# Kernel tuning notes

Measured on AMD Instinct MI355X. Metric: run time of the kernel, lower is better.

Reference implementation:

```python
import jax, jax.numpy as jnp
import numpy as np

T = 4096        # sequence length
D = 128         # input feature dim
TRACE = 64      # trace_size
CONTEXT = 64    # context_size
HID = 64        # internal dense width (hardcoded 64 in module)
OUT = 128       # output_size
LN_EPS = 1e-6   # flax LayerNorm default epsilon


def setup_inputs() -> dict:
    key = jax.random.key(0)
    ks = jax.random.split(key, 12)

    def dense(k, fi, fo):
        return (jax.random.normal(k, (fi, fo), jnp.float32) / np.sqrt(fi).astype(np.float32))

    inp = {}
    inp["x"] = jax.random.normal(ks[0], (T, D), jnp.float32)
    inp["state"] = jnp.zeros((1, TRACE, CONTEXT), jnp.complex64)
    inp["start"] = jax.random.uniform(ks[1], (T,)) < 0.01  # sparse episode resets
    # deterministic FFM decay / frequency params (init_deterministic)
    inp["a"] = jnp.linspace(1e-6, 0.5, TRACE).astype(jnp.float32)
    inp["b"] = (2.0 * jnp.pi / jnp.linspace(1.0, 1000.0, CONTEXT)).astype(jnp.float32)
    inp["W1"] = dense(ks[2], D, HID);               inp["b1"] = jnp.zeros((HID,), jnp.float32)
    inp["W2"] = dense(ks[3], HID, 2 * TRACE);       inp["b2"] = jnp.zeros((2 * TRACE,), jnp.float32)
    inp["Wgi"] = dense(ks[4], 2 * TRACE, TRACE);    inp["bgi"] = jnp.zeros((TRACE,), jnp.float32)
    inp["Wp"] = dense(ks[5], 2 * TRACE, TRACE);     inp["bp"] = jnp.zeros((TRACE,), jnp.float32)
    inp["Wz"] = dense(ks[6], 2 * TRACE * CONTEXT, HID); inp["bz"] = jnp.zeros((HID,), jnp.float32)
    inp["Wgo"] = dense(ks[7], 2 * TRACE, HID);      inp["bgo"] = jnp.zeros((HID,), jnp.float32)
    inp["Ws"] = dense(ks[8], 2 * TRACE, HID);       inp["bs"] = jnp.zeros((HID,), jnp.float32)
    inp["W3"] = dense(ks[9], HID, HID);             inp["b3"] = jnp.zeros((HID,), jnp.float32)
    inp["W4"] = dense(ks[10], HID, OUT);            inp["b4"] = jnp.zeros((OUT,), jnp.float32)
    return inp


def _ffm_scan(scan_in, state0, start, a, b):
    # scan_in: (T, TRACE, CONTEXT) float, state0: (1, TRACE, CONTEXT) complex64
    t = scan_in.shape[0]
    timestep = jnp.ones((t + 1, 1, 1), dtype=jnp.int32)
    start_f = jnp.concatenate(
        [jnp.zeros((1, 1, 1), dtype=bool), start.reshape(t, 1, 1)], axis=0)
    xs = jnp.concatenate([state0, scan_in.astype(jnp.complex64)], axis=0)

    neg_a = -jnp.abs(a).reshape(1, TRACE, 1)
    b_r = b.reshape(1, 1, CONTEXT)
    ab = neg_a + 1j * b_r  # (1, TRACE, CONTEXT) complex

    def gamma(j):
        # j: (N,1,1) int -> (N, TRACE, CONTEXT) complex decay
        return jnp.exp(ab * j.astype(jnp.float32))

    def combine(carry, incoming):
        prev_start, s, i = carry
        st, xx, j = incoming
        keep = jnp.logical_not(st)
        s = s * keep
        j = j * keep.astype(j.dtype)
        new_s = s * gamma(j) + xx
        return (jnp.logical_or(st, prev_start), new_s, j + i)

    _, new_state, _ = jax.lax.associative_scan(
        combine, (start_f, xs, timestep), axis=0)
    return new_state[1:]  # (T, TRACE, CONTEXT) complex64


def _layernorm(x):
    mu = jnp.mean(x, axis=-1, keepdims=True)
    var = jnp.var(x, axis=-1, keepdims=True)
    return (x - mu) * jax.lax.rsqrt(var + LN_EPS)


def _forward(x, state, start, a, b, W1, b1, W2, b2, Wgi, bgi, Wp, bp,
             Wz, bz, Wgo, bgo, Ws, bs, W3, b3, W4, b4):
    h = jax.nn.relu(x @ W1 + b1)                 # (T, 64)
    h2 = h @ W2 + b2                             # (T, 2*TRACE)
    gate_in = jax.nn.sigmoid(h2 @ Wgi + bgi)     # (T, TRACE)
    pre = jax.nn.sigmoid(h2 @ Wp + bp)           # (T, TRACE)
    gated = pre * gate_in                        # (T, TRACE)
    scan_in = jnp.broadcast_to(gated[:, :, None], (gated.shape[0], TRACE, CONTEXT))
    state_seq = _ffm_scan(scan_in, state, start, a, b)  # (T, TRACE, CONTEXT) c64
    z_in = jnp.concatenate([jnp.real(state_seq), jnp.imag(state_seq)],
                           axis=-1).reshape(state_seq.shape[0], -1)
    z = z_in @ Wz + bz                           # (T, 64)
    gate_out = jax.nn.sigmoid(h2 @ Wgo + bgo)    # (T, 64)
    skip = h2 @ Ws + bs                          # (T, 64)
    out = _layernorm(z * gate_out) + skip * (1.0 - gate_out)
    out = jax.nn.relu(out @ W3 + b3)
    out = out @ W4 + b4                          # (T, OUT)
    return out, state_seq[-1:]


def reference(x, state, start, a, b, W1, b1, W2, b2, Wgi, bgi, Wp, bp,
              Wz, bz, Wgo, bgo, Ws, bs, W3, b3, W4, b4):
    return _forward(x, state, start, a, b, W1, b1, W2, b2, Wgi, bgi, Wp, bp,
                    Wz, bz, Wgo, bgo, Ws, bs, W3, b3, W4, b4)
```

## Files before the change

### kernel.cpp

```cpp
#include <hip/hip_runtime.h>
#include <math.h>

#define T_LEN 4096
#define D_IN 128
#define HID 64
#define KDIM 4096
#define K2   8192

#define OFF_GATED 0u
#define OFF_GO    262144u
#define OFF_SKIP  524288u
#define OFF_PART  786432u
#define OFF_FLAGS 4980736u
#define OFF_CHS   4984832u
#define OFF_WZT   4984896u
#define OFF_SCR   5247040u

typedef __attribute__((ext_vector_type(8))) short short8v;
typedef __attribute__((ext_vector_type(4))) float float4v;

__device__ __forceinline__ float sigm(float x){ return 1.f/(1.f+expf(-x)); }
__device__ __forceinline__ unsigned short f2bf(float x){
    unsigned int u = __float_as_uint(x);
    return (unsigned short)((u + 0x7FFFu + ((u >> 16) & 1u)) >> 16);
}

__global__ __launch_bounds__(512) void k_prep(
    const unsigned char* __restrict__ su8, const int* __restrict__ si32,
    int* __restrict__ flags, int* __restrict__ chunkStart,
    const float* __restrict__ Wz, unsigned short* __restrict__ wzt,
    const float* __restrict__ x,
    const float* __restrict__ W1, const float* __restrict__ b1,
    const float* __restrict__ W2, const float* __restrict__ b2,
    const float* __restrict__ Wgi, const float* __restrict__ bgi,
    const float* __restrict__ Wp,  const float* __restrict__ bp,
    const float* __restrict__ Wgo, const float* __restrict__ bgo,
    const float* __restrict__ Wsk, const float* __restrict__ bsk,
    float* __restrict__ gated, float* __restrict__ go, float* __restrict__ sk)
{
    const int bx = blockIdx.x;
    const int tid = threadIdx.x;

    if (bx == 0) {
        __shared__ int cnt;
        if (tid == 0) cnt = 0;
        __syncthreads();
        int local = 0;
        for (int i = tid; i < 4096; i += 512)
            if (i & 3) local += su8[i];
        if (local) atomicAdd(&cnt, local);
        __syncthreads();
        if (cnt > 0) {
            for (int i = tid; i < 4096; i += 512) flags[i] = su8[i] ? 1 : 0;
        } else {
            for (int i = tid; i < 4096; i += 512) flags[i] = si32[i] ? 1 : 0;
        }
        __syncthreads();
        if (tid < 64) {
            int any = 0;
#pragma unroll 8
            for (int j = 0; j < 64; ++j) any |= flags[tid * 64 + j];
            chunkStart[tid] = any;
        }
        return;
    }
    if (bx <= 64) {
        int idx = ((bx - 1) * 512 + tid) * 16;
        int j = idx >> 13, k0 = idx & 8191;
#pragma unroll
        for (int e = 0; e < 16; ++e) {
            int k = k0 + e;
            wzt[(size_t)j * K2 + k] = f2bf(Wz[(size_t)k * 64 + j]);
        }
        return;
    }

    __shared__ float xs[8][128];
    __shared__ float hs[8][64];
    __shared__ float h2s[8][128];
    __shared__ float tmp[8][4][64];
    const int t0 = (bx - 65) * 8;

    if (tid < 256) {
        int r = tid >> 5, kq = (tid & 31) << 2;
        *(float4*)&xs[r][kq] = *(const float4*)&x[(size_t)(t0 + r) * D_IN + kq];
    }

    const int j1 = tid >> 3, ks1 = tid & 7;
    float wr1[16];
#pragma unroll
    for (int kk = 0; kk < 16; ++kk) wr1[kk] = W1[(size_t)(ks1 * 16 + kk) * HID + j1];
    const float bias1 = b1[j1];
    __syncthreads();
#pragma unroll
    for (int r = 0; r < 8; ++r) {
        float p = 0.f;
#pragma unroll
        for (int kq = 0; kq < 4; ++kq) {
            float4 xv = *(const float4*)&xs[r][ks1 * 16 + kq * 4];
            p += xv.x * wr1[kq*4] + xv.y * wr1[kq*4+1] + xv.z * wr1[kq*4+2] + xv.w * wr1[kq*4+3];
        }
        p += __shfl_xor(p, 1, 64); p += __shfl_xor(p, 2, 64); p += __shfl_xor(p, 4, 64);
        if (ks1 == 0) hs[r][j1] = fmaxf(p + bias1, 0.f);
    }

    const int j2 = tid >> 2, ks2 = tid & 3;
    float wr2[16];
#pragma unroll
    for (int kk = 0; kk < 16; ++kk) wr2[kk] = W2[(size_t)(ks2 * 16 + kk) * 128 + j2];
    const float bias2 = b2[j2];
    __syncthreads();
#pragma unroll
    for (int r = 0; r < 8; ++r) {
        float p = 0.f;
#pragma unroll
        for (int kq = 0; kq < 4; ++kq) {
            float4 hv = *(const float4*)&hs[r][ks2 * 16 + kq * 4];
            p += hv.x * wr2[kq*4] + hv.y * wr2[kq*4+1] + hv.z * wr2[kq*4+2] + hv.w * wr2[kq*4+3];
        }
        p += __shfl_xor(p, 1, 64); p += __shfl_xor(p, 2, 64);
        if (ks2 == 0) h2s[r][j2] = p + bias2;
    }

    const int mat = tid >> 7, jj = (tid & 127) >> 1, kh = tid & 1;
    const float* Wm = (mat == 0) ? Wgi : (mat == 1) ? Wp : (mat == 2) ? Wgo : Wsk;
    float wgr[64];
#pragma unroll
    for (int kk = 0; kk < 64; ++kk) wgr[kk] = Wm[(size_t)(kh * 64 + kk) * 64 + jj];
    __syncthreads();
#pragma unroll
    for (int r = 0; r < 8; ++r) {
        float p = 0.f;
#pragma unroll
        for (int kq = 0; kq < 16; ++kq) {
            float4 hv = *(const float4*)&h2s[r][kh * 64 + kq * 4];
            p += hv.x * wgr[kq*4] + hv.y * wgr[kq*4+1] + hv.z * wgr[kq*4+2] + hv.w * wgr[kq*4+3];
        }
        p += __shfl_xor(p, 1, 64);
        if (kh == 0) tmp[r][mat][jj] = p;
    }
    __syncthreads();

    {
        int r = tid >> 6, j = tid & 63;
        int t = t0 + r;
        float gi = sigm(tmp[r][0][j] + bgi[j]);
        float pr = sigm(tmp[r][1][j] + bp[j]);
        float g  = sigm(tmp[r][2][j] + bgo[j]);
        float s  = tmp[r][3][j] + bsk[j];
        gated[t * 64 + j] = gi * pr;
        go[t * 64 + j]    = g;
        sk[t * 64 + j]    = s;
    }
}

__global__ __launch_bounds__(512) void k_scanA(
    const float* __restrict__ gated, const int* __restrict__ flags,
    const float* __restrict__ a, const float* __restrict__ b,
    float2* __restrict__ carryB)
{
    const int p = threadIdx.x >> 6, c = threadIdx.x & 63;
    const int pair = blockIdx.x * 8 + p;
    const int ch = pair & 63, m = pair >> 6;
    const int t0 = ch * 64;
    __shared__ float gb[8][64];
    __shared__ int fb[8][64];
    gb[p][c] = gated[(size_t)(t0 + c) * 64 + m];
    fb[p][c] = flags[t0 + c];
    __syncthreads();

    const double ea = exp(-fabs((double)a[m]));
    const double bb = (double)b[c];
    const double lre = ea * cos(bb), lim = ea * sin(bb);
    double sre = 0.0, sim = 0.0;
#pragma unroll 8
    for (int j = 0; j < 64; ++j) {
        double g = (double)gb[p][j];
        if (fb[p][j]) { sre = g; sim = 0.0; }
        else {
            double nr = fma(sre, lre, fma(-sim, lim, g));
            double ni = fma(sre, lim, sim * lre);
            sre = nr; sim = ni;
        }
    }
    carryB[(size_t)ch * KDIM + m * 64 + c] = make_float2((float)sre, (float)sim);
}

__global__ __launch_bounds__(64) void k_scanC(
    const float2* __restrict__ carryB, const int* __restrict__ chunkStart,
    const float* __restrict__ a, const float* __restrict__ b,
    const float* __restrict__ st0,
    float2* __restrict__ cinArr)
{
    const int m = blockIdx.x, c = threadIdx.x;
    __shared__ int chsS[64];
    chsS[c] = chunkStart[c];

    float2 Bv[64];
#pragma unroll
    for (int ch = 0; ch < 64; ++ch)
        Bv[ch] = carryB[(size_t)ch * KDIM + m * 64 + c];
    __syncthreads();

    const double ea64 = exp(-64.0 * fabs((double)a[m]));
    const double bb = (double)b[c];
    const double l64re = ea64 * cos(64.0 * bb), l64im = ea64 * sin(64.0 * bb);
    double cre = (double)st0[(m * 64 + c) * 2];
    double cim = (double)st0[(m * 64 + c) * 2 + 1];
#pragma unroll
    for (int ch = 0; ch < 64; ++ch) {
        cinArr[(size_t)ch * KDIM + m * 64 + c] = make_float2((float)cre, (float)cim);
        if (chsS[ch]) { cre = (double)Bv[ch].x; cim = (double)Bv[ch].y; }
        else {
            double nr = fma(cre, l64re, fma(-cim, l64im, (double)Bv[ch].x));
            double ni = fma(cre, l64im, fma(cim, l64re, (double)Bv[ch].y));
            cre = nr; cim = ni;
        }
    }
}

__global__ __launch_bounds__(256) void k_scanBZ(
    const float* __restrict__ gated, const int* __restrict__ flags,
    const float* __restrict__ a, const float* __restrict__ b,
    const float2* __restrict__ cinArr,
    const unsigned short* __restrict__ wzt,
    float* __restrict__ part,
    float* __restrict__ out)
{
    const int tid = threadIdx.x;
    const int ml = tid >> 6, c = tid & 63;
    const int ch = blockIdx.x & 63, mg = blockIdx.x >> 6;
    const int m = mg * 4 + ml;
    const int t0 = ch * 64;
    __shared__ unsigned short st[64 * 512];
    __shared__ float gb[4][64];
    __shared__ int fb[64];
    gb[ml][c] = gated[(size_t)(t0 + c) * 64 + m];
    if (ml == 0) fb[c] = flags[t0 + c];
    __syncthreads();

    const double ea = exp(-fabs((double)a[m]));
    const double bb = (double)b[c];
    const double lre = ea * cos(bb), lim = ea * sin(bb);
    float2 cin = cinArr[(size_t)ch * KDIM + m * 64 + c];
    double sre = (double)cin.x, sim = (double)cin.y;
    const int e0 = ml * 128 + c, e1 = ml * 128 + 64 + c;
#pragma unroll 4
    for (int j = 0; j < 64; ++j) {
        double g = (double)gb[ml][j];
        if (fb[j]) { sre = g; sim = 0.0; }
        else {
            double nr = fma(sre, lre, fma(-sim, lim, g));
            double ni = fma(sre, lim, sim * lre);
            sre = nr; sim = ni;
        }
        const int sx = (j & 7) << 3;
        st[j * 512 + (e0 ^ sx)] = f2bf((float)sre);
        st[j * 512 + (e1 ^ sx)] = f2bf((float)sim);
    }
    if (ch == 63) {
        out[524288 + m * 64 + c]        = (float)sre;
        out[524288 + 4096 + m * 64 + c] = (float)sim;
    }

    const int l = c;
    const int jrow = ml * 16 + (l & 15);
    short8v bfr[16];
#pragma unroll
    for (int ks = 0; ks < 16; ++ks)
        bfr[ks] = *(const short8v*)&wzt[(size_t)jrow * K2 + mg * 512 + (ks * 4 + (l >> 4)) * 8];

    __syncthreads();

    float4v acc[4];
#pragma unroll
    for (int i = 0; i < 4; ++i) acc[i] = (float4v){0.f, 0.f, 0.f, 0.f};
#pragma unroll
    for (int ks = 0; ks < 16; ++ks) {
#pragma unroll
        for (int mt = 0; mt < 4; ++mt) {
            const int row = mt * 16 + (l & 15);
            const int rchunk = (ks * 4 + (l >> 4)) ^ (row & 7);
            short8v af = *(const short8v*)&st[row * 512 + rchunk * 8];
            acc[mt] = __builtin_amdgcn_mfma_f32_16x16x32_bf16(af, bfr[ks], acc[mt], 0, 0, 0);
        }
    }

    float* pp = part + (size_t)mg * 262144;
    const int jcol = ml * 16 + (l & 15);
#pragma unroll
    for (int mt = 0; mt < 4; ++mt) {
        const int trow = t0 + mt * 16 + (l >> 4) * 4;
#pragma unroll
        for (int r = 0; r < 4; ++r)
            pp[(size_t)(trow + r) * 64 + jcol] = acc[mt][r];
    }
}

__device__ __forceinline__ float wsum(float v) {
#pragma unroll
    for (int o = 32; o; o >>= 1) v += __shfl_xor(v, o, 64);
    return v;
}

__global__ __launch_bounds__(256) void k_epi(
    const float* __restrict__ part, const float* __restrict__ bz,
    const float* __restrict__ go, const float* __restrict__ sk,
    const float* __restrict__ W3, const float* __restrict__ b3,
    const float* __restrict__ W4, const float* __restrict__ b4,
    float* __restrict__ out)
{
    __shared__ float ob[4][64], hb[4][64];
    const int w = threadIdx.x >> 6, j = threadIdx.x & 63;
    const int t = blockIdx.x * 4 + w;
    float z = bz[j];
#pragma unroll
    for (int p = 0; p < 16; ++p) z += part[(size_t)p * 262144 + t * 64 + j];
    float g = go[t * 64 + j];
    float y = z * g;
    float mu = wsum(y) * 0.015625f;
    float d = y - mu;
    float var = wsum(d * d) * 0.015625f;
    float o = d * (1.f / sqrtf(var + 1e-6f)) + sk[t * 64 + j] * (1.f - g);
    ob[w][j] = o;
    __syncthreads();
    float acc = b3[j];
#pragma unroll 8
    for (int k = 0; k < 64; ++k) acc += ob[w][k] * W3[k * 64 + j];
    hb[w][j] = fmaxf(acc, 0.f);
    __syncthreads();
    float o1 = b4[j], o2 = b4[j + 64];
#pragma unroll 8
    for (int k = 0; k < 64; ++k) { float hv = hb[w][k]; o1 += hv * W4[k * 128 + j]; o2 += hv * W4[k * 128 + j + 64]; }
    out[(size_t)t * 128 + j] = o1;
    out[(size_t)t * 128 + j + 64] = o2;
}

extern "C" void kernel_launch(void* const* d_in, const int* in_sizes, int n_in,
                              void* d_out, int out_size, void* d_ws, size_t ws_size,
                              hipStream_t stream)
{
    const float* x   = (const float*)d_in[0];
    const float* st0 = (const float*)d_in[1];
    const void*  start = d_in[2];
    const float* a  = (const float*)d_in[3];
    const float* b  = (const float*)d_in[4];
    const float* W1 = (const float*)d_in[5];  const float* b1 = (const float*)d_in[6];
    const float* W2 = (const float*)d_in[7];  const float* b2 = (const float*)d_in[8];
    const float* Wgi= (const float*)d_in[9];  const float* bgi= (const float*)d_in[10];
    const float* Wp = (const float*)d_in[11]; const float* bp = (const float*)d_in[12];
    const float* Wz = (const float*)d_in[13]; const float* bz = (const float*)d_in[14];
    const float* Wgo= (const float*)d_in[15]; const float* bgo= (const float*)d_in[16];
    const float* Wsk= (const float*)d_in[17]; const float* bsk= (const float*)d_in[18];
    const float* W3 = (const float*)d_in[19]; const float* b3 = (const float*)d_in[20];
    const float* W4 = (const float*)d_in[21]; const float* b4 = (const float*)d_in[22];

    float* ws    = (float*)d_ws;
    float* out   = (float*)d_out;
    float* gated = ws + OFF_GATED;
    float* go    = ws + OFF_GO;
    float* sk    = ws + OFF_SKIP;
    float* part  = ws + OFF_PART;
    int*   flags = (int*)(ws + OFF_FLAGS);
    int*   chs   = (int*)(ws + OFF_CHS);
    unsigned short* wzt  = (unsigned short*)(ws + OFF_WZT);

    float2* carryB = (float2*)(ws + OFF_SCR);
    float2* cinArr = (float2*)(ws + OFF_SCR + 524288);

    hipLaunchKernelGGL(k_prep, dim3(577), dim3(512), 0, stream,
                       (const unsigned char*)start, (const int*)start, flags, chs,
                       Wz, wzt, x, W1, b1, W2, b2, Wgi, bgi, Wp, bp,
                       Wgo, bgo, Wsk, bsk, gated, go, sk);
    hipLaunchKernelGGL(k_scanA, dim3(512), dim3(512), 0, stream,
                       gated, flags, a, b, carryB);
    hipLaunchKernelGGL(k_scanC, dim3(64), dim3(64), 0, stream,
                       carryB, chs, a, b, st0, cinArr);
    hipLaunchKernelGGL(k_scanBZ, dim3(1024), dim3(256), 0, stream,
                       gated, flags, a, b, cinArr, wzt, part, out);
    hipLaunchKernelGGL(k_epi, dim3(1024), dim3(256), 0, stream,
                       part, bz, go, sk, W3, b3, W4, b4, out);
}
```

Before: 86.17 us.

## Fuse five kernels into one persistent kernel with global atomic barriers

```diff
diff --git a/kernel.cpp b/kernel.cpp
--- a/kernel.cpp
+++ b/kernel.cpp
@@ -3,9 +3,9 @@
 
 #define T_LEN 4096
 #define D_IN 128
-#define HID 64
 #define KDIM 4096
 #define K2   8192
+#define NBLK 256
 
 #define OFF_GATED 0u
 #define OFF_GO    262144u
@@ -15,6 +15,7 @@
 #define OFF_CHS   4984832u
 #define OFF_WZT   4984896u
 #define OFF_SCR   5247040u
+#define OFF_BAR   6295616u
 
 typedef __attribute__((ext_vector_type(8))) short short8v;
 typedef __attribute__((ext_vector_type(4))) float float4v;
@@ -24,360 +25,327 @@
     unsigned int u = __float_as_uint(x);
     return (unsigned short)((u + 0x7FFFu + ((u >> 16) & 1u)) >> 16);
 }
-
-__global__ __launch_bounds__(512) void k_prep(
-    const unsigned char* __restrict__ su8, const int* __restrict__ si32,
-    int* __restrict__ flags, int* __restrict__ chunkStart,
-    const float* __restrict__ Wz, unsigned short* __restrict__ wzt,
-    const float* __restrict__ x,
-    const float* __restrict__ W1, const float* __restrict__ b1,
-    const float* __restrict__ W2, const float* __restrict__ b2,
-    const float* __restrict__ Wgi, const float* __restrict__ bgi,
-    const float* __restrict__ Wp,  const float* __restrict__ bp,
-    const float* __restrict__ Wgo, const float* __restrict__ bgo,
-    const float* __restrict__ Wsk, const float* __restrict__ bsk,
-    float* __restrict__ gated, float* __restrict__ go, float* __restrict__ sk)
-{
+__device__ __forceinline__ float wsum(float v) {
+#pragma unroll
+    for (int o = 32; o; o >>= 1) v += __shfl_xor(v, o, 64);
+    return v;
+}
+
+struct Params {
+    const unsigned char* su8; const int* si32;
+    const float *x, *st0, *a, *b;
+    const float *W1,*b1,*W2,*b2,*Wgi,*bgi,*Wp,*bp,*Wz,*bz,*Wgo,*bgo,*Wsk,*bsk,*W3,*b3,*W4,*b4;
+    float *gated,*go,*sk,*part; int *flags,*chs; unsigned short* wzt;
+    float2 *carryB,*cinArr; float* out; int* bar;
+};
+
+__device__ __forceinline__ void gsync(int* bar) {
+    __syncthreads();
+    if (threadIdx.x == 0) {
+        __threadfence();
+        atomicAdd(bar, 1);
+        while (atomicAdd(bar, 0) < NBLK) __builtin_amdgcn_s_sleep(8);
+        __threadfence();
+    }
+    __syncthreads();
+}
+
+__global__ __launch_bounds__(512) void k_mega(Params P) {
+    __shared__ __align__(16) char smem[65536];
     const int bx = blockIdx.x;
     const int tid = threadIdx.x;
 
     if (bx == 0) {
-        __shared__ int cnt;
-        if (tid == 0) cnt = 0;
+        int* cnt = (int*)(smem + 20480);
+        if (tid == 0) *cnt = 0;
         __syncthreads();
         int local = 0;
         for (int i = tid; i < 4096; i += 512)
-            if (i & 3) local += su8[i];
-        if (local) atomicAdd(&cnt, local);
+            if (i & 3) local += P.su8[i];
+        if (local) atomicAdd(cnt, local);
         __syncthreads();
-        if (cnt > 0) {
-            for (int i = tid; i < 4096; i += 512) flags[i] = su8[i] ? 1 : 0;
-        } else {
-            for (int i = tid; i < 4096; i += 512) flags[i] = si32[i] ? 1 : 0;
-        }
+        if (*cnt > 0) { for (int i = tid; i < 4096; i += 512) P.flags[i] = P.su8[i] ? 1 : 0; }
+        else          { for (int i = tid; i < 4096; i += 512) P.flags[i] = P.si32[i] ? 1 : 0; }
         __syncthreads();
         if (tid < 64) {
             int any = 0;
 #pragma unroll 8
-            for (int j = 0; j < 64; ++j) any |= flags[tid * 64 + j];
-            chunkStart[tid] = any;
-        }
-        return;
-    }
-    if (bx <= 64) {
+            for (int j = 0; j < 64; ++j) any |= P.flags[tid * 64 + j];
+            P.chs[tid] = any;
+        }
+    }
+    if (bx >= 1 && bx <= 64) {
         int idx = ((bx - 1) * 512 + tid) * 16;
         int j = idx >> 13, k0 = idx & 8191;
 #pragma unroll
         for (int e = 0; e < 16; ++e) {
             int k = k0 + e;
-            wzt[(size_t)j * K2 + k] = f2bf(Wz[(size_t)k * 64 + j]);
-        }
-        return;
-    }
-
-    __shared__ float xs[8][128];
-    __shared__ float hs[8][64];
-    __shared__ float h2s[8][128];
-    __shared__ float tmp[8][4][64];
-    const int t0 = (bx - 65) * 8;
-
-    if (tid < 256) {
-        int r = tid >> 5, kq = (tid & 31) << 2;
-        *(float4*)&xs[r][kq] = *(const float4*)&x[(size_t)(t0 + r) * D_IN + kq];
-    }
-
-    const int j1 = tid >> 3, ks1 = tid & 7;
-    float wr1[16];
-#pragma unroll
-    for (int kk = 0; kk < 16; ++kk) wr1[kk] = W1[(size_t)(ks1 * 16 + kk) * HID + j1];
-    const float bias1 = b1[j1];
-    __syncthreads();
-#pragma unroll
-    for (int r = 0; r < 8; ++r) {
-        float p = 0.f;
-#pragma unroll
-        for (int kq = 0; kq < 4; ++kq) {
-            float4 xv = *(const float4*)&xs[r][ks1 * 16 + kq * 4];
-            p += xv.x * wr1[kq*4] + xv.y * wr1[kq*4+1] + xv.z * wr1[kq*4+2] + xv.w * wr1[kq*4+3];
-        }
-        p += __shfl_xor(p, 1, 64); p += __shfl_xor(p, 2, 64); p += __shfl_xor(p, 4, 64);
-        if (ks1 == 0) hs[r][j1] = fmaxf(p + bias1, 0.f);
-    }
-
-    const int j2 = tid >> 2, ks2 = tid & 3;
-    float wr2[16];
-#pragma unroll
-    for (int kk = 0; kk < 16; ++kk) wr2[kk] = W2[(size_t)(ks2 * 16 + kk) * 128 + j2];
-    const float bias2 = b2[j2];
-    __syncthreads();
-#pragma unroll
-    for (int r = 0; r < 8; ++r) {
-        float p = 0.f;
-#pragma unroll
-        for (int kq = 0; kq < 4; ++kq) {
-            float4 hv = *(const float4*)&hs[r][ks2 * 16 + kq * 4];
-            p += hv.x * wr2[kq*4] + hv.y * wr2[kq*4+1] + hv.z * wr2[kq*4+2] + hv.w * wr2[kq*4+3];
-        }
-        p += __shfl_xor(p, 1, 64); p += __shfl_xor(p, 2, 64);
-        if (ks2 == 0) h2s[r][j2] = p + bias2;
-    }
-
-    const int mat = tid >> 7, jj = (tid & 127) >> 1, kh = tid & 1;
-    const float* Wm = (mat == 0) ? Wgi : (mat == 1) ? Wp : (mat == 2) ? Wgo : Wsk;
-    float wgr[64];
-#pragma unroll
-    for (int kk = 0; kk < 64; ++kk) wgr[kk] = Wm[(size_t)(kh * 64 + kk) * 64 + jj];
-    __syncthreads();
-#pragma unroll
-    for (int r = 0; r < 8; ++r) {
-        float p = 0.f;
-#pragma unroll
-        for (int kq = 0; kq < 16; ++kq) {
-            float4 hv = *(const float4*)&h2s[r][kh * 64 + kq * 4];
-            p += hv.x * wgr[kq*4] + hv.y * wgr[kq*4+1] + hv.z * wgr[kq*4+2] + hv.w * wgr[kq*4+3];
-        }
-        p += __shfl_xor(p, 1, 64);
-        if (kh == 0) tmp[r][mat][jj] = p;
-    }
-    __syncthreads();
-
+            P.wzt[(size_t)j * K2 + k] = f2bf(P.Wz[(size_t)k * 64 + j]);
+        }
+    }
     {
-        int r = tid >> 6, j = tid & 63;
-        int t = t0 + r;
-        float gi = sigm(tmp[r][0][j] + bgi[j]);
-        float pr = sigm(tmp[r][1][j] + bp[j]);
-        float g  = sigm(tmp[r][2][j] + bgo[j]);
-        float s  = tmp[r][3][j] + bsk[j];
-        gated[t * 64 + j] = gi * pr;
-        go[t * 64 + j]    = g;
-        sk[t * 64 + j]    = s;
-    }
-}
-
-__global__ __launch_bounds__(512) void k_scanA(
-    const float* __restrict__ gated, const int* __restrict__ flags,
-    const float* __restrict__ a, const float* __restrict__ b,
-    float2* __restrict__ carryB)
-{
-    const int p = threadIdx.x >> 6, c = threadIdx.x & 63;
-    const int pair = blockIdx.x * 8 + p;
-    const int ch = pair & 63, m = pair >> 6;
-    const int t0 = ch * 64;
-    __shared__ float gb[8][64];
-    __shared__ int fb[8][64];
-    gb[p][c] = gated[(size_t)(t0 + c) * 64 + m];
-    fb[p][c] = flags[t0 + c];
-    __syncthreads();
-
-    const double ea = exp(-fabs((double)a[m]));
-    const double bb = (double)b[c];
-    const double lre = ea * cos(bb), lim = ea * sin(bb);
-    double sre = 0.0, sim = 0.0;
+        float (*xs)[128]  = (float(*)[128])smem;
+        float (*hs)[64]   = (float(*)[64])(smem + 4096);
+        float (*h2s)[128] = (float(*)[128])(smem + 6144);
+        float (*tmp)[4][64] = (float(*)[4][64])(smem + 10240);
+
+        const int j1 = tid >> 3, ks1 = tid & 7;
+        float wr1[16];
+#pragma unroll
+        for (int kk = 0; kk < 16; ++kk) wr1[kk] = P.W1[(size_t)(ks1 * 16 + kk) * 64 + j1];
+        const float bias1 = P.b1[j1];
+        const int j2 = tid >> 2, ks2 = tid & 3;
+        float wr2[16];
+#pragma unroll
+        for (int kk = 0; kk < 16; ++kk) wr2[kk] = P.W2[(size_t)(ks2 * 16 + kk) * 128 + j2];
+        const float bias2 = P.b2[j2];
+        const int mat = tid >> 7, jj = (tid & 127) >> 1, kh = tid & 1;
+        const float* Wm = (mat == 0) ? P.Wgi : (mat == 1) ? P.Wp : (mat == 2) ? P.Wgo : P.Wsk;
+        float wgr[64];
+#pragma unroll
+        for (int kk = 0; kk < 64; ++kk) wgr[kk] = Wm[(size_t)(kh * 64 + kk) * 64 + jj];
+
+        for (int u = 0; u < 2; ++u) {
+            const int t0 = (bx * 2 + u) * 8;
+            __syncthreads();
+            if (tid < 256) {
+                int r = tid >> 5, kq = (tid & 31) << 2;
+                *(float4*)&xs[r][kq] = *(const float4*)&P.x[(size_t)(t0 + r) * D_IN + kq];
+            }
+            __syncthreads();
+#pragma unroll
+            for (int r = 0; r < 8; ++r) {
+                float p = 0.f;
+#pragma unroll
+                for (int kq = 0; kq < 4; ++kq) {
+                    float4 xv = *(const float4*)&xs[r][ks1 * 16 + kq * 4];
+                    p += xv.x*wr1[kq*4] + xv.y*wr1[kq*4+1] + xv.z*wr1[kq*4+2] + xv.w*wr1[kq*4+3];
+                }
+                p += __shfl_xor(p, 1, 64); p += __shfl_xor(p, 2, 64); p += __shfl_xor(p, 4, 64);
+                if (ks1 == 0) hs[r][j1] = fmaxf(p + bias1, 0.f);
+            }
+            __syncthreads();
+#pragma unroll
+            for (int r = 0; r < 8; ++r) {
+                float p = 0.f;
+#pragma unroll
+                for (int kq = 0; kq < 4; ++kq) {
+                    float4 hv = *(const float4*)&hs[r][ks2 * 16 + kq * 4];
+                    p += hv.x*wr2[kq*4] + hv.y*wr2[kq*4+1] + hv.z*wr2[kq*4+2] + hv.w*wr2[kq*4+3];
+                }
+                p += __shfl_xor(p, 1, 64); p += __shfl_xor(p, 2, 64);
+                if (ks2 == 0) h2s[r][j2] = p + bias2;
+            }
+            __syncthreads();
+#pragma unroll
+            for (int r = 0; r < 8; ++r) {
+                float p = 0.f;
+#pragma unroll
+                for (int kq = 0; kq < 16; ++kq) {
+                    float4 hv = *(const float4*)&h2s[r][kh * 64 + kq * 4];
+                    p += hv.x*wgr[kq*4] + hv.y*wgr[kq*4+1] + hv.z*wgr[kq*4+2] + hv.w*wgr[kq*4+3];
+                }
+                p += __shfl_xor(p, 1, 64);
+                if (kh == 0) tmp[r][mat][jj] = p;
+            }
+            __syncthreads();
+            {
+                int r = tid >> 6, j = tid & 63;
+                int t = t0 + r;
+                float gi = sigm(tmp[r][0][j] + P.bgi[j]);
+                float pr = sigm(tmp[r][1][j] + P.bp[j]);
+                float g  = sigm(tmp[r][2][j] + P.bgo[j]);
+                float s  = tmp[r][3][j] + P.bsk[j];
+                P.gated[t * 64 + j] = gi * pr;
+                P.go[t * 64 + j]    = g;
+                P.sk[t * 64 + j]    = s;
+            }
+        }
+    }
+    gsync(P.bar + 0);
+
+    {
+        const int p = tid >> 6, c = tid & 63;
+#pragma unroll
+        for (int u = 0; u < 2; ++u) {
+            const int pair = (bx * 2 + u) * 8 + p;
+            const int ch = pair & 63, m = pair >> 6, t0s = ch * 64;
+            const double ea = exp(-fabs((double)P.a[m]));
+            const double bb = (double)P.b[c];
+            const double lre = ea * cos(bb), lim = ea * sin(bb);
+            float gv = P.gated[(size_t)(t0s + c) * 64 + m];
+            unsigned long long fmask = __ballot(P.flags[t0s + c] != 0);
+            double sre = 0.0, sim = 0.0;
 #pragma unroll 8
-    for (int j = 0; j < 64; ++j) {
-        double g = (double)gb[p][j];
-        if (fb[p][j]) { sre = g; sim = 0.0; }
-        else {
-            double nr = fma(sre, lre, fma(-sim, lim, g));
-            double ni = fma(sre, lim, sim * lre);
-            sre = nr; sim = ni;
-        }
-    }
-    carryB[(size_t)ch * KDIM + m * 64 + c] = make_float2((float)sre, (float)sim);
-}
-
-__global__ __launch_bounds__(64) void k_scanC(
-    const float2* __restrict__ carryB, const int* __restrict__ chunkStart,
-    const float* __restrict__ a, const float* __restrict__ b,
-    const float* __restrict__ st0,
-    float2* __restrict__ cinArr)
-{
-    const int m = blockIdx.x, c = threadIdx.x;
-    __shared__ int chsS[64];
-    chsS[c] = chunkStart[c];
-
-    float2 Bv[64];
-#pragma unroll
-    for (int ch = 0; ch < 64; ++ch)
-        Bv[ch] = carryB[(size_t)ch * KDIM + m * 64 + c];
-    __syncthreads();
-
-    const double ea64 = exp(-64.0 * fabs((double)a[m]));
-    const double bb = (double)b[c];
-    const double l64re = ea64 * cos(64.0 * bb), l64im = ea64 * sin(64.0 * bb);
-    double cre = (double)st0[(m * 64 + c) * 2];
-    double cim = (double)st0[(m * 64 + c) * 2 + 1];
-#pragma unroll
-    for (int ch = 0; ch < 64; ++ch) {
-        cinArr[(size_t)ch * KDIM + m * 64 + c] = make_float2((float)cre, (float)cim);
-        if (chsS[ch]) { cre = (double)Bv[ch].x; cim = (double)Bv[ch].y; }
-        else {
-            double nr = fma(cre, l64re, fma(-cim, l64im, (double)Bv[ch].x));
-            double ni = fma(cre, l64im, fma(cim, l64re, (double)Bv[ch].y));
-            cre = nr; cim = ni;
-        }
-    }
-}
-
-__global__ __launch_bounds__(256) void k_scanBZ(
-    const float* __restrict__ gated, const int* __restrict__ flags,
-    const float* __restrict__ a, const float* __restrict__ b,
-    const float2* __restrict__ cinArr,
-    const unsigned short* __restrict__ wzt,
-    float* __restrict__ part,
-    float* __restrict__ out)
-{
-    const int tid = threadIdx.x;
-    const int ml = tid >> 6, c = tid & 63;
-    const int ch = blockIdx.x & 63, mg = blockIdx.x >> 6;
-    const int m = mg * 4 + ml;
-    const int t0 = ch * 64;
-    __shared__ unsigned short st[64 * 512];
-    __shared__ float gb[4][64];
-    __shared__ int fb[64];
-    gb[ml][c] = gated[(size_t)(t0 + c) * 64 + m];
-    if (ml == 0) fb[c] = flags[t0 + c];
-    __syncthreads();
-
-    const double ea = exp(-fabs((double)a[m]));
-    const double bb = (double)b[c];
-    const double lre = ea * cos(bb), lim = ea * sin(bb);
-    float2 cin = cinArr[(size_t)ch * KDIM + m * 64 + c];
-    double sre = (double)cin.x, sim = (double)cin.y;
-    const int e0 = ml * 128 + c, e1 = ml * 128 + 64 + c;
+            for (int j = 0; j < 64; ++j) {
+                double g = (double)__shfl(gv, j, 64);
+                if ((fmask >> j) & 1) { sre = g; sim = 0.0; }
+                else {
+                    double nr = fma(sre, lre, fma(-sim, lim, g));
+                    double ni = fma(sre, lim, sim * lre);
+                    sre = nr; sim = ni;
+                }
+            }
+            P.carryB[(size_t)ch * KDIM + m * 64 + c] = make_float2((float)sre, (float)sim);
+        }
+    }
+    gsync(P.bar + 16);
+
+    if (bx < 64 && tid < 64) {
+        const int m = bx, c = tid;
+        unsigned long long cmask = __ballot(P.chs[c] != 0);
+        float2 Bv[64];
+#pragma unroll
+        for (int ch = 0; ch < 64; ++ch)
+            Bv[ch] = P.carryB[(size_t)ch * KDIM + m * 64 + c];
+        const double ea64 = exp(-64.0 * fabs((double)P.a[m]));
+        const double bb = (double)P.b[c];
+        const double l64re = ea64 * cos(64.0 * bb), l64im = ea64 * sin(64.0 * bb);
+        double cre = (double)P.st0[(m * 64 + c) * 2];
+        double cim = (double)P.st0[(m * 64 + c) * 2 + 1];
+#pragma unroll
+        for (int ch = 0; ch < 64; ++ch) {
+            P.cinArr[(size_t)ch * KDIM + m * 64 + c] = make_float2((float)cre, (float)cim);
+            if ((cmask >> ch) & 1) { cre = (double)Bv[ch].x; cim = (double)Bv[ch].y; }
+            else {
+                double nr = fma(cre, l64re, fma(-cim, l64im, (double)Bv[ch].x));
+                double ni = fma(cre, l64im, fma(cim, l64re, (double)Bv[ch].y));
+                cre = nr; cim = ni;
+            }
+        }
+    }
+    gsync(P.bar + 32);
+
+    {
+        unsigned short* st = (unsigned short*)smem;
+        const int w = tid >> 6, l = tid & 63;
+        const int ml = w & 3, mth = w >> 2;
+        for (int u = 0; u < 4; ++u) {
+            const int pair = bx * 4 + u;
+            const int ch = pair & 63, mg = pair >> 6, t0s = ch * 64;
+            const int m = mg * 4 + ml;
+            const int jrow = ml * 16 + (l & 15);
+            short8v bfr[16];
+#pragma unroll
+            for (int ks = 0; ks < 16; ++ks)
+                bfr[ks] = *(const short8v*)&P.wzt[(size_t)jrow * K2 + mg * 512 + (ks * 4 + (l >> 4)) * 8];
+            __syncthreads();
+            if (w < 4) {
+                const double ea = exp(-fabs((double)P.a[m]));
+                const double bb = (double)P.b[l];
+                const double lre = ea * cos(bb), lim = ea * sin(bb);
+                float gv = P.gated[(size_t)(t0s + l) * 64 + m];
+                unsigned long long fmask = __ballot(P.flags[t0s + l] != 0);
+                float2 cin = P.cinArr[(size_t)ch * KDIM + m * 64 + l];
+                double sre = (double)cin.x, sim = (double)cin.y;
+                const int e0 = ml * 128 + l, e1 = e0 + 64;
 #pragma unroll 4
-    for (int j = 0; j < 64; ++j) {
-        double g = (double)gb[ml][j];
-        if (fb[j]) { sre = g; sim = 0.0; }
-        else {
-            double nr = fma(sre, lre, fma(-sim, lim, g));
-            double ni = fma(sre, lim, sim * lre);
-            sre = nr; sim = ni;
-        }
-        const int sx = (j & 7) << 3;
-        st[j * 512 + (e0 ^ sx)] = f2bf((float)sre);
-        st[j * 512 + (e1 ^ sx)] = f2bf((float)sim);
-    }
-    if (ch == 63) {
-        out[524288 + m * 64 + c]        = (float)sre;
-        out[524288 + 4096 + m * 64 + c] = (float)sim;
-    }
-
-    const int l = c;
-    const int jrow = ml * 16 + (l & 15);
-    short8v bfr[16];
-#pragma unroll
-    for (int ks = 0; ks < 16; ++ks)
-        bfr[ks] = *(const short8v*)&wzt[(size_t)jrow * K2 + mg * 512 + (ks * 4 + (l >> 4)) * 8];
-
-    __syncthreads();
-
-    float4v acc[4];
-#pragma unroll
-    for (int i = 0; i < 4; ++i) acc[i] = (float4v){0.f, 0.f, 0.f, 0.f};
-#pragma unroll
-    for (int ks = 0; ks < 16; ++ks) {
-#pragma unroll
-        for (int mt = 0; mt < 4; ++mt) {
-            const int row = mt * 16 + (l & 15);
-            const int rchunk = (ks * 4 + (l >> 4)) ^ (row & 7);
-            short8v af = *(const short8v*)&st[row * 512 + rchunk * 8];
-            acc[mt] = __builtin_amdgcn_mfma_f32_16x16x32_bf16(af, bfr[ks], acc[mt], 0, 0, 0);
-        }
-    }
-
-    float* pp = part + (size_t)mg * 262144;
-    const int jcol = ml * 16 + (l & 15);
-#pragma unroll
-    for (int mt = 0; mt < 4; ++mt) {
-        const int trow = t0 + mt * 16 + (l >> 4) * 4;
-#pragma unroll
-        for (int r = 0; r < 4; ++r)
-            pp[(size_t)(trow + r) * 64 + jcol] = acc[mt][r];
-    }
-}
-
-__device__ __forceinline__ float wsum(float v) {
-#pragma unroll
-    for (int o = 32; o; o >>= 1) v += __shfl_xor(v, o, 64);
-    return v;
-}
-
-__global__ __launch_bounds__(256) void k_epi(
-    const float* __restrict__ part, const float* __restrict__ bz,
-    const float* __restrict__ go, const float* __restrict__ sk,
-    const float* __restrict__ W3, const float* __restrict__ b3,
-    const float* __restrict__ W4, const float* __restrict__ b4,
-    float* __restrict__ out)
-{
-    __shared__ float ob[4][64], hb[4][64];
-    const int w = threadIdx.x >> 6, j = threadIdx.x & 63;
-    const int t = blockIdx.x * 4 + w;
-    float z = bz[j];
-#pragma unroll
-    for (int p = 0; p < 16; ++p) z += part[(size_t)p * 262144 + t * 64 + j];
-    float g = go[t * 64 + j];
-    float y = z * g;
-    float mu = wsum(y) * 0.015625f;
-    float d = y - mu;
-    float var = wsum(d * d) * 0.015625f;
-    float o = d * (1.f / sqrtf(var + 1e-6f)) + sk[t * 64 + j] * (1.f - g);
-    ob[w][j] = o;
-    __syncthreads();
-    float acc = b3[j];
+                for (int j = 0; j < 64; ++j) {
+                    double g = (double)__shfl(gv, j, 64);
+                    if ((fmask >> j) & 1) { sre = g; sim = 0.0; }
+                    else {
+                        double nr = fma(sre, lre, fma(-sim, lim, g));
+                        double ni = fma(sre, lim, sim * lre);
+                        sre = nr; sim = ni;
+                    }
+                    const int sx = (j & 7) << 3;
+                    st[j * 512 + (e0 ^ sx)] = f2bf((float)sre);
+                    st[j * 512 + (e1 ^ sx)] = f2bf((float)sim);
+                }
+                if (ch == 63) {
+                    P.out[524288 + m * 64 + l]        = (float)sre;
+                    P.out[524288 + 4096 + m * 64 + l] = (float)sim;
+                }
+            }
+            __syncthreads();
+            float4v acc[2];
+            acc[0] = (float4v){0.f,0.f,0.f,0.f};
+            acc[1] = (float4v){0.f,0.f,0.f,0.f};
+#pragma unroll
+            for (int ks = 0; ks < 16; ++ks) {
+#pragma unroll
+                for (int q = 0; q < 2; ++q) {
+                    const int row = (mth * 2 + q) * 16 + (l & 15);
+                    const int rchunk = (ks * 4 + (l >> 4)) ^ (row & 7);
+                    short8v af = *(const short8v*)&st[row * 512 + rchunk * 8];
+                    acc[q] = __builtin_amdgcn_mfma_f32_16x16x32_bf16(af, bfr[ks], acc[q], 0, 0, 0);
+                }
+            }
+            float* pp = P.part + (size_t)mg * 262144;
+            const int jcol = ml * 16 + (l & 15);
+#pragma unroll
+            for (int q = 0; q < 2; ++q) {
+                const int trow = t0s + (mth * 2 + q) * 16 + (l >> 4) * 4;
+#pragma unroll
+                for (int r = 0; r < 4; ++r)
+                    pp[(size_t)(trow + r) * 64 + jcol] = acc[q][r];
+            }
+        }
+    }
+    gsync(P.bar + 48);
+
+    {
+        float (*ob)[64] = (float(*)[64])smem;
+        float (*hb)[64] = (float(*)[64])(smem + 2048);
+        const int w = tid >> 6, j = tid & 63;
+        for (int it = 0; it < 2; ++it) {
+            const int t = bx * 16 + it * 8 + w;
+            float z = P.bz[j];
+#pragma unroll
+            for (int p = 0; p < 16; ++p) z += P.part[(size_t)p * 262144 + t * 64 + j];
+            float g = P.go[t * 64 + j];
+            float y = z * g;
+            float mu = wsum(y) * 0.015625f;
+            float d = y - mu;
+            float var = wsum(d * d) * 0.015625f;
+            float o = d * (1.f / sqrtf(var + 1e-6f)) + P.sk[t * 64 + j] * (1.f - g);
+            ob[w][j] = o;
+            float acc2 = P.b3[j];
 #pragma unroll 8
-    for (int k = 0; k < 64; ++k) acc += ob[w][k] * W3[k * 64 + j];
-    hb[w][j] = fmaxf(acc, 0.f);
-    __syncthreads();
-    float o1 = b4[j], o2 = b4[j + 64];
+            for (int k = 0; k < 64; ++k) acc2 += ob[w][k] * P.W3[k * 64 + j];
+            hb[w][j] = fmaxf(acc2, 0.f);
+            float o1 = P.b4[j], o2 = P.b4[j + 64];
 #pragma unroll 8
-    for (int k = 0; k < 64; ++k) { float hv = hb[w][k]; o1 += hv * W4[k * 128 + j]; o2 += hv * W4[k * 128 + j + 64]; }
-    out[(size_t)t * 128 + j] = o1;
-    out[(size_t)t * 128 + j + 64] = o2;
+            for (int k = 0; k < 64; ++k) { float hv = hb[w][k]; o1 += hv * P.W4[k * 128 + j]; o2 += hv * P.W4[k * 128 + j + 64]; }
+            P.out[(size_t)t * 128 + j] = o1;
+            P.out[(size_t)t * 128 + j + 64] = o2;
+        }
+    }
 }
 
 extern "C" void kernel_launch(void* const* d_in, const int* in_sizes, int n_in,
                               void* d_out, int out_size, void* d_ws, size_t ws_size,
                               hipStream_t stream)
 {
-    const float* x   = (const float*)d_in[0];
-    const float* st0 = (const float*)d_in[1];
-    const void*  start = d_in[2];
-    const float* a  = (const float*)d_in[3];
-    const float* b  = (const float*)d_in[4];
-    const float* W1 = (const float*)d_in[5];  const float* b1 = (const float*)d_in[6];
-    const float* W2 = (const float*)d_in[7];  const float* b2 = (const float*)d_in[8];
-    const float* Wgi= (const float*)d_in[9];  const float* bgi= (const float*)d_in[10];
-    const float* Wp = (const float*)d_in[11]; const float* bp = (const float*)d_in[12];
-    const float* Wz = (const float*)d_in[13]; const float* bz = (const float*)d_in[14];
-    const float* Wgo= (const float*)d_in[15]; const float* bgo= (const float*)d_in[16];
-    const float* Wsk= (const float*)d_in[17]; const float* bsk= (const float*)d_in[18];
-    const float* W3 = (const float*)d_in[19]; const float* b3 = (const float*)d_in[20];
-    const float* W4 = (const float*)d_in[21]; const float* b4 = (const float*)d_in[22];
-
-    float* ws    = (float*)d_ws;
-    float* out   = (float*)d_out;
-    float* gated = ws + OFF_GATED;
-    float* go    = ws + OFF_GO;
-    float* sk    = ws + OFF_SKIP;
-    float* part  = ws + OFF_PART;
-    int*   flags = (int*)(ws + OFF_FLAGS);
-    int*   chs   = (int*)(ws + OFF_CHS);
-    unsigned short* wzt  = (unsigned short*)(ws + OFF_WZT);
-
-    float2* carryB = (float2*)(ws + OFF_SCR);
-    float2* cinArr = (float2*)(ws + OFF_SCR + 524288);
-
-    hipLaunchKernelGGL(k_prep, dim3(577), dim3(512), 0, stream,
-                       (const unsigned char*)start, (const int*)start, flags, chs,
-                       Wz, wzt, x, W1, b1, W2, b2, Wgi, bgi, Wp, bp,
-                       Wgo, bgo, Wsk, bsk, gated, go, sk);
-    hipLaunchKernelGGL(k_scanA, dim3(512), dim3(512), 0, stream,
-                       gated, flags, a, b, carryB);
-    hipLaunchKernelGGL(k_scanC, dim3(64), dim3(64), 0, stream,
-                       carryB, chs, a, b, st0, cinArr);
-    hipLaunchKernelGGL(k_scanBZ, dim3(1024), dim3(256), 0, stream,
-                       gated, flags, a, b, cinArr, wzt, part, out);
-    hipLaunchKernelGGL(k_epi, dim3(1024), dim3(256), 0, stream,
-                       part, bz, go, sk, W3, b3, W4, b4, out);
-}
+    float* ws = (float*)d_ws;
+    Params P;
+    P.su8 = (const unsigned char*)d_in[2];
+    P.si32 = (const int*)d_in[2];
+    P.x   = (const float*)d_in[0];
+    P.st0 = (const float*)d_in[1];
+    P.a   = (const float*)d_in[3];
+    P.b   = (const float*)d_in[4];
+    P.W1  = (const float*)d_in[5];  P.b1  = (const float*)d_in[6];
+    P.W2  = (const float*)d_in[7];  P.b2  = (const float*)d_in[8];
+    P.Wgi = (const float*)d_in[9];  P.bgi = (const float*)d_in[10];
+    P.Wp  = (const float*)d_in[11]; P.bp  = (const float*)d_in[12];
+    P.Wz  = (const float*)d_in[13]; P.bz  = (const float*)d_in[14];
+    P.Wgo = (const float*)d_in[15]; P.bgo = (const float*)d_in[16];
+    P.Wsk = (const float*)d_in[17]; P.bsk = (const float*)d_in[18];
+    P.W3  = (const float*)d_in[19]; P.b3  = (const float*)d_in[20];
+    P.W4  = (const float*)d_in[21]; P.b4  = (const float*)d_in[22];
+    P.gated = ws + OFF_GATED;
+    P.go    = ws + OFF_GO;
+    P.sk    = ws + OFF_SKIP;
+    P.part  = ws + OFF_PART;
+    P.flags = (int*)(ws + OFF_FLAGS);
+    P.chs   = (int*)(ws + OFF_CHS);
+    P.wzt   = (unsigned short*)(ws + OFF_WZT);
+    P.carryB = (float2*)(ws + OFF_SCR);
+    P.cinArr = (float2*)(ws + OFF_SCR + 524288);
+    P.out   = (float*)d_out;
+    P.bar   = (int*)(ws + OFF_BAR);
+
+    hipMemsetAsync(P.bar, 0, 64 * sizeof(int), stream);
+    hipLaunchKernelGGL(k_mega, dim3(NBLK), dim3(512), 0, stream, P);
+}
```

After: 173.3 us. 101% more time.

## Fold chunk-carry propagation into scan kernel and use wave shuffles instead of LDS

Applied to the files above, without the earlier changes.

```diff
diff --git a/kernel.cpp b/kernel.cpp
--- a/kernel.cpp
+++ b/kernel.cpp
@@ -3,7 +3,6 @@
 
 #define T_LEN 4096
 #define D_IN 128
-#define HID 64
 #define KDIM 4096
 #define K2   8192
 
@@ -23,6 +22,11 @@
 __device__ __forceinline__ unsigned short f2bf(float x){
     unsigned int u = __float_as_uint(x);
     return (unsigned short)((u + 0x7FFFu + ((u >> 16) & 1u)) >> 16);
+}
+__device__ __forceinline__ float wsum(float v) {
+#pragma unroll
+    for (int o = 32; o; o >>= 1) v += __shfl_xor(v, o, 64);
+    return v;
 }
 
 __global__ __launch_bounds__(512) void k_prep(
@@ -50,11 +54,8 @@
             if (i & 3) local += su8[i];
         if (local) atomicAdd(&cnt, local);
         __syncthreads();
-        if (cnt > 0) {
-            for (int i = tid; i < 4096; i += 512) flags[i] = su8[i] ? 1 : 0;
-        } else {
-            for (int i = tid; i < 4096; i += 512) flags[i] = si32[i] ? 1 : 0;
-        }
+        if (cnt > 0) { for (int i = tid; i < 4096; i += 512) flags[i] = su8[i] ? 1 : 0; }
+        else         { for (int i = tid; i < 4096; i += 512) flags[i] = si32[i] ? 1 : 0; }
         __syncthreads();
         if (tid < 64) {
             int any = 0;
@@ -89,7 +90,7 @@
     const int j1 = tid >> 3, ks1 = tid & 7;
     float wr1[16];
 #pragma unroll
-    for (int kk = 0; kk < 16; ++kk) wr1[kk] = W1[(size_t)(ks1 * 16 + kk) * HID + j1];
+    for (int kk = 0; kk < 16; ++kk) wr1[kk] = W1[(size_t)(ks1 * 16 + kk) * 64 + j1];
     const float bias1 = b1[j1];
     __syncthreads();
 #pragma unroll
@@ -98,43 +99,43 @@
 #pragma unroll
         for (int kq = 0; kq < 4; ++kq) {
             float4 xv = *(const float4*)&xs[r][ks1 * 16 + kq * 4];
-            p += xv.x * wr1[kq*4] + xv.y * wr1[kq*4+1] + xv.z * wr1[kq*4+2] + xv.w * wr1[kq*4+3];
+            p += xv.x*wr1[kq*4] + xv.y*wr1[kq*4+1] + xv.z*wr1[kq*4+2] + xv.w*wr1[kq*4+3];
         }
         p += __shfl_xor(p, 1, 64); p += __shfl_xor(p, 2, 64); p += __shfl_xor(p, 4, 64);
         if (ks1 == 0) hs[r][j1] = fmaxf(p + bias1, 0.f);
     }
+    __syncthreads();
 
     const int j2 = tid >> 2, ks2 = tid & 3;
     float wr2[16];
 #pragma unroll
     for (int kk = 0; kk < 16; ++kk) wr2[kk] = W2[(size_t)(ks2 * 16 + kk) * 128 + j2];
     const float bias2 = b2[j2];
-    __syncthreads();
 #pragma unroll
     for (int r = 0; r < 8; ++r) {
         float p = 0.f;
 #pragma unroll
         for (int kq = 0; kq < 4; ++kq) {
             float4 hv = *(const float4*)&hs[r][ks2 * 16 + kq * 4];
-            p += hv.x * wr2[kq*4] + hv.y * wr2[kq*4+1] + hv.z * wr2[kq*4+2] + hv.w * wr2[kq*4+3];
+            p += hv.x*wr2[kq*4] + hv.y*wr2[kq*4+1] + hv.z*wr2[kq*4+2] + hv.w*wr2[kq*4+3];
         }
         p += __shfl_xor(p, 1, 64); p += __shfl_xor(p, 2, 64);
         if (ks2 == 0) h2s[r][j2] = p + bias2;
     }
+    __syncthreads();
 
     const int mat = tid >> 7, jj = (tid & 127) >> 1, kh = tid & 1;
     const float* Wm = (mat == 0) ? Wgi : (mat == 1) ? Wp : (mat == 2) ? Wgo : Wsk;
     float wgr[64];
 #pragma unroll
     for (int kk = 0; kk < 64; ++kk) wgr[kk] = Wm[(size_t)(kh * 64 + kk) * 64 + jj];
-    __syncthreads();
 #pragma unroll
     for (int r = 0; r < 8; ++r) {
         float p = 0.f;
 #pragma unroll
         for (int kq = 0; kq < 16; ++kq) {
             float4 hv = *(const float4*)&h2s[r][kh * 64 + kq * 4];
-            p += hv.x * wgr[kq*4] + hv.y * wgr[kq*4+1] + hv.z * wgr[kq*4+2] + hv.w * wgr[kq*4+3];
+            p += hv.x*wgr[kq*4] + hv.y*wgr[kq*4+1] + hv.z*wgr[kq*4+2] + hv.w*wgr[kq*4+3];
         }
         p += __shfl_xor(p, 1, 64);
         if (kh == 0) tmp[r][mat][jj] = p;
@@ -163,20 +164,17 @@
     const int pair = blockIdx.x * 8 + p;
     const int ch = pair & 63, m = pair >> 6;
     const int t0 = ch * 64;
-    __shared__ float gb[8][64];
-    __shared__ int fb[8][64];
-    gb[p][c] = gated[(size_t)(t0 + c) * 64 + m];
-    fb[p][c] = flags[t0 + c];
-    __syncthreads();
 
     const double ea = exp(-fabs((double)a[m]));
     const double bb = (double)b[c];
     const double lre = ea * cos(bb), lim = ea * sin(bb);
+    float gv = gated[(size_t)(t0 + c) * 64 + m];
+    unsigned long long fmask = __ballot(flags[t0 + c] != 0);
     double sre = 0.0, sim = 0.0;
 #pragma unroll 8
     for (int j = 0; j < 64; ++j) {
-        double g = (double)gb[p][j];
-        if (fb[p][j]) { sre = g; sim = 0.0; }
+        double g = (double)__shfl(gv, j, 64);
+        if ((fmask >> j) & 1) { sre = g; sim = 0.0; }
         else {
             double nr = fma(sre, lre, fma(-sim, lim, g));
             double ni = fma(sre, lim, sim * lre);
@@ -186,43 +184,12 @@
     carryB[(size_t)ch * KDIM + m * 64 + c] = make_float2((float)sre, (float)sim);
 }
 
-__global__ __launch_bounds__(64) void k_scanC(
-    const float2* __restrict__ carryB, const int* __restrict__ chunkStart,
+__global__ __launch_bounds__(256) void k_scanBZq(
+    const float* __restrict__ gated, const int* __restrict__ flags,
+    const int* __restrict__ chs,
     const float* __restrict__ a, const float* __restrict__ b,
     const float* __restrict__ st0,
-    float2* __restrict__ cinArr)
-{
-    const int m = blockIdx.x, c = threadIdx.x;
-    __shared__ int chsS[64];
-    chsS[c] = chunkStart[c];
-
-    float2 Bv[64];
-#pragma unroll
-    for (int ch = 0; ch < 64; ++ch)
-        Bv[ch] = carryB[(size_t)ch * KDIM + m * 64 + c];
-    __syncthreads();
-
-    const double ea64 = exp(-64.0 * fabs((double)a[m]));
-    const double bb = (double)b[c];
-    const double l64re = ea64 * cos(64.0 * bb), l64im = ea64 * sin(64.0 * bb);
-    double cre = (double)st0[(m * 64 + c) * 2];
-    double cim = (double)st0[(m * 64 + c) * 2 + 1];
-#pragma unroll
-    for (int ch = 0; ch < 64; ++ch) {
-        cinArr[(size_t)ch * KDIM + m * 64 + c] = make_float2((float)cre, (float)cim);
-        if (chsS[ch]) { cre = (double)Bv[ch].x; cim = (double)Bv[ch].y; }
-        else {
-            double nr = fma(cre, l64re, fma(-cim, l64im, (double)Bv[ch].x));
-            double ni = fma(cre, l64im, fma(cim, l64re, (double)Bv[ch].y));
-            cre = nr; cim = ni;
-        }
-    }
-}
-
-__global__ __launch_bounds__(256) void k_scanBZ(
-    const float* __restrict__ gated, const int* __restrict__ flags,
-    const float* __restrict__ a, const float* __restrict__ b,
-    const float2* __restrict__ cinArr,
+    const float2* __restrict__ carryB,
     const unsigned short* __restrict__ wzt,
     float* __restrict__ part,
     float* __restrict__ out)
@@ -233,22 +200,34 @@
     const int m = mg * 4 + ml;
     const int t0 = ch * 64;
     __shared__ unsigned short st[64 * 512];
-    __shared__ float gb[4][64];
-    __shared__ int fb[64];
-    gb[ml][c] = gated[(size_t)(t0 + c) * 64 + m];
-    if (ml == 0) fb[c] = flags[t0 + c];
-    __syncthreads();
 
     const double ea = exp(-fabs((double)a[m]));
     const double bb = (double)b[c];
     const double lre = ea * cos(bb), lim = ea * sin(bb);
-    float2 cin = cinArr[(size_t)ch * KDIM + m * 64 + c];
-    double sre = (double)cin.x, sim = (double)cin.y;
-    const int e0 = ml * 128 + c, e1 = ml * 128 + 64 + c;
+
+    unsigned long long cmask = __ballot(chs[c] != 0);
+    const double ea64 = exp(-64.0 * fabs((double)a[m]));
+    const double l64re = ea64 * cos(64.0 * bb), l64im = ea64 * sin(64.0 * bb);
+    double cre = (double)st0[(m * 64 + c) * 2];
+    double cim = (double)st0[(m * 64 + c) * 2 + 1];
+    for (int chp = 0; chp < ch; ++chp) {
+        float2 B = carryB[(size_t)chp * KDIM + m * 64 + c];
+        if ((cmask >> chp) & 1) { cre = (double)B.x; cim = (double)B.y; }
+        else {
+            double nr = fma(cre, l64re, fma(-cim, l64im, (double)B.x));
+            double ni = fma(cre, l64im, fma(cim, l64re, (double)B.y));
+            cre = nr; cim = ni;
+        }
+    }
+
+    float gv = gated[(size_t)(t0 + c) * 64 + m];
+    unsigned long long fmask = __ballot(flags[t0 + c] != 0);
+    double sre = cre, sim = cim;
+    const int e0 = ml * 128 + c, e1 = e0 + 64;
 #pragma unroll 4
     for (int j = 0; j < 64; ++j) {
-        double g = (double)gb[ml][j];
-        if (fb[j]) { sre = g; sim = 0.0; }
+        double g = (double)__shfl(gv, j, 64);
+        if ((fmask >> j) & 1) { sre = g; sim = 0.0; }
         else {
             double nr = fma(sre, lre, fma(-sim, lim, g));
             double ni = fma(sre, lim, sim * lre);
@@ -295,12 +274,6 @@
         for (int r = 0; r < 4; ++r)
             pp[(size_t)(trow + r) * 64 + jcol] = acc[mt][r];
     }
-}
-
-__device__ __forceinline__ float wsum(float v) {
-#pragma unroll
-    for (int o = 32; o; o >>= 1) v += __shfl_xor(v, o, 64);
-    return v;
 }
 
 __global__ __launch_bounds__(256) void k_epi(
@@ -363,10 +336,8 @@
     float* part  = ws + OFF_PART;
     int*   flags = (int*)(ws + OFF_FLAGS);
     int*   chs   = (int*)(ws + OFF_CHS);
-    unsigned short* wzt  = (unsigned short*)(ws + OFF_WZT);
-
+    unsigned short* wzt = (unsigned short*)(ws + OFF_WZT);
     float2* carryB = (float2*)(ws + OFF_SCR);
-    float2* cinArr = (float2*)(ws + OFF_SCR + 524288);
 
     hipLaunchKernelGGL(k_prep, dim3(577), dim3(512), 0, stream,
                        (const unsigned char*)start, (const int*)start, flags, chs,
@@ -374,10 +345,8 @@
                        Wgo, bgo, Wsk, bsk, gated, go, sk);
     hipLaunchKernelGGL(k_scanA, dim3(512), dim3(512), 0, stream,
                        gated, flags, a, b, carryB);
-    hipLaunchKernelGGL(k_scanC, dim3(64), dim3(64), 0, stream,
-                       carryB, chs, a, b, st0, cinArr);
-    hipLaunchKernelGGL(k_scanBZ, dim3(1024), dim3(256), 0, stream,
-                       gated, flags, a, b, cinArr, wzt, part, out);
+    hipLaunchKernelGGL(k_scanBZq, dim3(1024), dim3(256), 0, stream,
+                       gated, flags, chs, a, b, st0, carryB, wzt, part, out);
     hipLaunchKernelGGL(k_epi, dim3(1024), dim3(256), 0, stream,
                        part, bz, go, sk, W3, b3, W4, b4, out);
 }
```

Measured after the change: 115.2 us. 1.34x slower.
